# Kernel optimization log

Measured on AMD Instinct MI355X. Metric: run time of the kernel, lower is better.

Reference implementation:

```python
import jax, jax.numpy as jnp
import numpy as np

B = 131072
D = 512


def setup_inputs() -> dict:
    key = jax.random.key(0)
    kx, kL, kb, kc = jax.random.split(key, 4)
    x = jax.random.normal(kx, (B, D), dtype=jnp.float32)
    L = jax.random.normal(kL, (D, D), dtype=jnp.float32)
    b = jax.random.normal(kb, (D,), dtype=jnp.float32)
    c = jax.random.normal(kc, (1,), dtype=jnp.float32)
    return {"x": x, "L": L, "b": b, "c": c}


def reference(x, L, b, c):
    # y = diag(x L L' x') + x b + c == sum((x @ L)**2, -1) + x @ b + c
    # Avoids the naive O(B^2 D) GEMM and O(B^2) intermediate.
    xL = x @ L                      # [B, D]
    quad = jnp.sum(xL * xL, axis=-1)  # [B]
    y = quad + x @ b + c            # [B] (c broadcasts from [1])
    return y[:, None]               # [B, 1]
```

## Files before the change

### kernel.cpp

```cpp
#include <hip/hip_runtime.h>
#include <stdint.h>

#define D_DIM   512
#define BM      64
#define BK      32
#define THREADS 256
#define NBLOCKS 2048

typedef __attribute__((ext_vector_type(8))) __bf16 bf16x8;
typedef __attribute__((ext_vector_type(4))) float  f32x4;

__device__ __forceinline__ unsigned short f32_to_bf16_rne(float f) {
    uint32_t u = __builtin_bit_cast(uint32_t, f);
    u += 0x7FFFu + ((u >> 16) & 1u);
    return (unsigned short)(u >> 16);
}

__global__ void prep_lt(const float* __restrict__ L, unsigned short* __restrict__ Ltf) {
    int o = blockIdx.x * 256 + threadIdx.x;
    #pragma unroll
    for (int i = 0; i < 4; ++i) {
        int idx  = o + i * 65536;
        int e    = idx & 7;
        int l    = (idx >> 3) & 63;
        int tile = idx >> 9;
        int ntg  = tile & 31;
        int ks   = tile >> 5;
        int n    = ntg * 16 + (l & 15);
        int k    = ks * 32 + (l >> 4) * 8 + e;
        Ltf[idx] = f32_to_bf16_rne(L[k * 512 + n]);
    }
}

__global__ __launch_bounds__(THREADS, 2)
void psd_main(const float* __restrict__ x, const unsigned short* __restrict__ Ltf,
              const float* __restrict__ b, const float* __restrict__ c,
              float* __restrict__ out) {
    __shared__ __align__(16) float As[3][BM * BK];
    __shared__ __align__(16) float bsh[D_DIM];
    __shared__ float wpart[4][BM];
    __shared__ float bpart[BM];

    const int t    = threadIdx.x;
    const int w    = t >> 6;
    const int lane = t & 63;
    const int g    = lane >> 4;
    const int ln   = lane & 15;
    const int r8   = lane >> 3;
    const int u8   = lane & 7;

    char* AsB  = (char*)&As[0][0];
    char* bshB = (char*)&bsh[0];
    const char* xB = (const char*)x + (size_t)blockIdx.x * (BM * 2048);

    const unsigned short* LtW = Ltf + (size_t)w * 4096 + (size_t)lane * 8;

    f32x4 acc[4][8];
    #pragma unroll
    for (int m = 0; m < 4; ++m)
        #pragma unroll
        for (int nt = 0; nt < 8; ++nt)
            acc[m][nt] = (f32x4){0.f, 0.f, 0.f, 0.f};
    float bacc = 0.f;

#define STAGE(QOFF, SL)                                                                  \
    {                                                                                    \
        char* ldsw = AsB + (SL) * 8192 + w * 2048;                                       \
        _Pragma("unroll")                                                                \
        for (int j = 0; j < 2; ++j) {                                                    \
            const int row = w * 16 + j * 8 + r8;                                         \
            const char* gsrc = xB + (size_t)row * 2048 + (QOFF)                          \
                             + ((u8 ^ (row & 7)) << 4);                                  \
            __builtin_amdgcn_global_load_lds(                                            \
                (const __attribute__((address_space(1))) void*)gsrc,                     \
                (__attribute__((address_space(3))) void*)(ldsw + j * 1024), 16, 0, 0);   \
        }                                                                                \
    }

#define COMPUTE(RB)                                                                      \
    {                                                                                    \
        _Pragma("unroll")                                                                \
        for (int m = 0; m < 4; ++m) {                                                    \
            const int row = m * 16 + ln;                                                 \
            const int cb  = g * 2;                                                       \
            f32x4 f0 = *(const f32x4*)((RB) + row * 128 + (((cb    ) ^ (row & 7)) << 4));\
            f32x4 f1 = *(const f32x4*)((RB) + row * 128 + (((cb + 1) ^ (row & 7)) << 4));\
            bf16x8 a;                                                                    \
            a[0] = (__bf16)f0[0]; a[1] = (__bf16)f0[1];                                  \
            a[2] = (__bf16)f0[2]; a[3] = (__bf16)f0[3];                                  \
            a[4] = (__bf16)f1[0]; a[5] = (__bf16)f1[1];                                  \
            a[6] = (__bf16)f1[2]; a[7] = (__bf16)f1[3];                                  \
            _Pragma("unroll")                                                            \
            for (int nt = 0; nt < 8; ++nt)                                               \
                acc[m][nt] = __builtin_amdgcn_mfma_f32_16x16x32_bf16(a, bfr[nt], acc[m][nt], 0, 0, 0); \
        }                                                                                \
    }

#define XB(RB, BOFF)                                                                     \
    {                                                                                    \
        const int row = t >> 2;                                                          \
        const int rsw = row & 7;                                                         \
        _Pragma("unroll")                                                                \
        for (int i = 0; i < 2; ++i) {                                                    \
            const int unit = (t & 3) * 2 + i;                                            \
            f32x4 xv = *(const f32x4*)((RB) + row * 128 + ((unit ^ rsw) << 4));          \
            f32x4 bv = *(const f32x4*)(bshB + (BOFF) + unit * 16);                       \
            bacc += xv[0] * bv[0] + xv[1] * bv[1] + xv[2] * bv[2] + xv[3] * bv[3];       \
        }                                                                                \
    }

    if (t < 128) {
        const char* gsrc = (const char*)b + (size_t)t * 16;
        __builtin_amdgcn_global_load_lds(
            (const __attribute__((address_space(1))) void*)gsrc,
            (__attribute__((address_space(3))) void*)(bshB + t * 16), 16, 0, 0);
    }
    STAGE(0, 0)
    STAGE(128, 1)
    asm volatile("s_waitcnt vmcnt(2)" ::: "memory");
    __builtin_amdgcn_s_barrier();

    int sl   = 0;
    int qoff = 2 * 128;
    int boff = 0;
    const unsigned short* Lp = LtW;

    #pragma unroll 1
    for (int q = 0; q < 14; ++q) {
        bf16x8 bfr[8];
        #pragma unroll
        for (int nt = 0; nt < 8; ++nt)
            bfr[nt] = *(const bf16x8*)(Lp + nt * 512);
        __builtin_amdgcn_sched_barrier(0);

        int sls = sl + 2; if (sls >= 3) sls -= 3;
        STAGE(qoff, sls)

        const char* rb = AsB + sl * 8192;
        COMPUTE(rb)
        XB(rb, boff)

        asm volatile("s_waitcnt lgkmcnt(0)" ::: "memory");
        asm volatile("s_waitcnt vmcnt(2)" ::: "memory");
        __builtin_amdgcn_s_barrier();

        if (++sl == 3) sl = 0;
        qoff += 128;
        boff += 128;
        Lp   += 16384;
    }

    {
        bf16x8 bfr[8];
        #pragma unroll
        for (int nt = 0; nt < 8; ++nt)
            bfr[nt] = *(const bf16x8*)(Lp + nt * 512);
        const char* rb = AsB + 2 * 8192;
        COMPUTE(rb)
        XB(rb, 14 * 128)
        asm volatile("s_waitcnt lgkmcnt(0)" ::: "memory");
        asm volatile("s_waitcnt vmcnt(0)" ::: "memory");
        __builtin_amdgcn_s_barrier();
    }
    {
        bf16x8 bfr[8];
        #pragma unroll
        for (int nt = 0; nt < 8; ++nt)
            bfr[nt] = *(const bf16x8*)(Lp + 16384 + nt * 512);
        const char* rb = AsB;
        COMPUTE(rb)
        XB(rb, 15 * 128)
    }

#undef STAGE
#undef COMPUTE
#undef XB

    #pragma unroll
    for (int m = 0; m < 4; ++m) {
        #pragma unroll
        for (int r = 0; r < 4; ++r) {
            float s = 0.f;
            #pragma unroll
            for (int nt = 0; nt < 8; ++nt) { float vv = acc[m][nt][r]; s += vv * vv; }
            s += __shfl_xor(s, 1);
            s += __shfl_xor(s, 2);
            s += __shfl_xor(s, 4);
            s += __shfl_xor(s, 8);
            if (ln == 0) wpart[w][m * 16 + g * 4 + r] = s;
        }
    }

    {
        float s = bacc;
        s += __shfl_xor(s, 1);
        s += __shfl_xor(s, 2);
        if ((lane & 3) == 0) bpart[t >> 2] = s;
    }
    __syncthreads();

    if (t < BM) {
        float y = c[0] + bpart[t]
                + wpart[0][t] + wpart[1][t] + wpart[2][t] + wpart[3][t];
        out[(size_t)blockIdx.x * BM + t] = y;
    }
}

extern "C" void kernel_launch(void* const* d_in, const int* in_sizes, int n_in,
                              void* d_out, int out_size, void* d_ws, size_t ws_size,
                              hipStream_t stream) {
    const float* x = (const float*)d_in[0];
    const float* L = (const float*)d_in[1];
    const float* b = (const float*)d_in[2];
    const float* c = (const float*)d_in[3];
    float* out = (float*)d_out;
    unsigned short* Ltf = (unsigned short*)d_ws;

    prep_lt<<<256, 256, 0, stream>>>(L, Ltf);
    psd_main<<<NBLOCKS, THREADS, 0, stream>>>(x, Ltf, b, c, out);
}
```

Measured before the change: 100.7 us.

## Convert x tiles to bf16 once into a shared ring and software-pipeline L loads

Each K-tile of x is now converted from fp32 to bf16 a single time by a cooperative pass, fused with the x·b dot product, and written into a swizzled double-buffered bf16 LDS ring. The MFMA loop then reads bf16 fragments directly instead of every wave re-reading and re-converting fp32 rows. L fragment loads are split into halves and prefetched one stage ahead, and the x staging is deepened to three tiles in flight. This removes redundant conversion ALU work and LDS traffic. It adds more LDS, hand-tuned waitcnt values that must match the load counts, and a longer unrolled prologue and epilogue.

```diff
diff --git a/kernel.cpp b/kernel.cpp
--- a/kernel.cpp
+++ b/kernel.cpp
@@ -3,7 +3,6 @@
 
 #define D_DIM   512
 #define BM      64
-#define BK      32
 #define THREADS 256
 #define NBLOCKS 2048
 
@@ -36,7 +35,8 @@
 void psd_main(const float* __restrict__ x, const unsigned short* __restrict__ Ltf,
               const float* __restrict__ b, const float* __restrict__ c,
               float* __restrict__ out) {
-    __shared__ __align__(16) float As[3][BM * BK];
+    __shared__ __align__(16) float pad[3][BM * 32];
+    __shared__ __align__(16) unsigned short ringb[2][BM * 32];
     __shared__ __align__(16) float bsh[D_DIM];
     __shared__ float wpart[4][BM];
     __shared__ float bpart[BM];
@@ -48,11 +48,13 @@
     const int ln   = lane & 15;
     const int r8   = lane >> 3;
     const int u8   = lane & 7;
-
-    char* AsB  = (char*)&As[0][0];
+    const int crow = t >> 2;
+    const int ccg  = t & 3;
+
+    char* padB = (char*)&pad[0][0];
+    char* rngB = (char*)&ringb[0][0];
     char* bshB = (char*)&bsh[0];
     const char* xB = (const char*)x + (size_t)blockIdx.x * (BM * 2048);
-
     const unsigned short* LtW = Ltf + (size_t)w * 4096 + (size_t)lane * 8;
 
     f32x4 acc[4][8];
@@ -63,118 +65,142 @@
             acc[m][nt] = (f32x4){0.f, 0.f, 0.f, 0.f};
     float bacc = 0.f;
 
-#define STAGE(QOFF, SL)                                                                  \
-    {                                                                                    \
-        char* ldsw = AsB + (SL) * 8192 + w * 2048;                                       \
+#define STAGE(K, SOFF)                                                                   \
+    {                                                                                    \
+        char* ldsw = padB + (SOFF) + w * 2048;                                           \
         _Pragma("unroll")                                                                \
         for (int j = 0; j < 2; ++j) {                                                    \
             const int row = w * 16 + j * 8 + r8;                                         \
-            const char* gsrc = xB + (size_t)row * 2048 + (QOFF)                          \
-                             + ((u8 ^ (row & 7)) << 4);                                  \
+            const char* gsrc = xB + (size_t)row * 2048 + (K) * 128 + ((u8 ^ r8) << 4);   \
             __builtin_amdgcn_global_load_lds(                                            \
                 (const __attribute__((address_space(1))) void*)gsrc,                     \
                 (__attribute__((address_space(3))) void*)(ldsw + j * 1024), 16, 0, 0);   \
         }                                                                                \
     }
 
-#define COMPUTE(RB)                                                                      \
+#define CVT_XB(K, COFF, ROFF)                                                            \
+    {                                                                                    \
+        const char* ps = padB + (COFF);                                                  \
+        f32x4 e0 = *(const f32x4*)(ps + crow * 128 + (((ccg * 2    ) ^ (crow & 7)) << 4)); \
+        f32x4 e1 = *(const f32x4*)(ps + crow * 128 + (((ccg * 2 + 1) ^ (crow & 7)) << 4)); \
+        f32x4 b0 = *(const f32x4*)(bshB + (K) * 128 + ccg * 32);                         \
+        f32x4 b1 = *(const f32x4*)(bshB + (K) * 128 + ccg * 32 + 16);                    \
+        bacc += e0[0]*b0[0] + e0[1]*b0[1] + e0[2]*b0[2] + e0[3]*b0[3]                    \
+              + e1[0]*b1[0] + e1[1]*b1[1] + e1[2]*b1[2] + e1[3]*b1[3];                   \
+        bf16x8 hv;                                                                       \
+        hv[0]=(__bf16)e0[0]; hv[1]=(__bf16)e0[1]; hv[2]=(__bf16)e0[2]; hv[3]=(__bf16)e0[3]; \
+        hv[4]=(__bf16)e1[0]; hv[5]=(__bf16)e1[1]; hv[6]=(__bf16)e1[2]; hv[7]=(__bf16)e1[3]; \
+        *(bf16x8*)(rngB + (ROFF) + crow * 64 + ((ccg ^ (crow & 3)) << 4)) = hv;          \
+    }
+
+#define LOADB(DST, Q, H)                                                                 \
+    {                                                                                    \
+        _Pragma("unroll")                                                                \
+        for (int i = 0; i < 4; ++i)                                                      \
+            (DST)[i] = *(const bf16x8*)(LtW + (size_t)(Q) * 16384 + ((H) * 4 + i) * 512); \
+    }
+
+#define COMPUTE_H(ROFF, BS, NB)                                                          \
     {                                                                                    \
         _Pragma("unroll")                                                                \
         for (int m = 0; m < 4; ++m) {                                                    \
             const int row = m * 16 + ln;                                                 \
-            const int cb  = g * 2;                                                       \
-            f32x4 f0 = *(const f32x4*)((RB) + row * 128 + (((cb    ) ^ (row & 7)) << 4));\
-            f32x4 f1 = *(const f32x4*)((RB) + row * 128 + (((cb + 1) ^ (row & 7)) << 4));\
-            bf16x8 a;                                                                    \
-            a[0] = (__bf16)f0[0]; a[1] = (__bf16)f0[1];                                  \
-            a[2] = (__bf16)f0[2]; a[3] = (__bf16)f0[3];                                  \
-            a[4] = (__bf16)f1[0]; a[5] = (__bf16)f1[1];                                  \
-            a[6] = (__bf16)f1[2]; a[7] = (__bf16)f1[3];                                  \
+            bf16x8 a = *(const bf16x8*)(rngB + (ROFF) + row * 64 + ((g ^ (row & 3)) << 4)); \
             _Pragma("unroll")                                                            \
-            for (int nt = 0; nt < 8; ++nt)                                               \
-                acc[m][nt] = __builtin_amdgcn_mfma_f32_16x16x32_bf16(a, bfr[nt], acc[m][nt], 0, 0, 0); \
+            for (int nt = 0; nt < 4; ++nt)                                               \
+                acc[m][(NB) + nt] = __builtin_amdgcn_mfma_f32_16x16x32_bf16(a, (BS)[nt], acc[m][(NB) + nt], 0, 0, 0); \
         }                                                                                \
     }
 
-#define XB(RB, BOFF)                                                                     \
-    {                                                                                    \
-        const int row = t >> 2;                                                          \
-        const int rsw = row & 7;                                                         \
-        _Pragma("unroll")                                                                \
-        for (int i = 0; i < 2; ++i) {                                                    \
-            const int unit = (t & 3) * 2 + i;                                            \
-            f32x4 xv = *(const f32x4*)((RB) + row * 128 + ((unit ^ rsw) << 4));          \
-            f32x4 bv = *(const f32x4*)(bshB + (BOFF) + unit * 16);                       \
-            bacc += xv[0] * bv[0] + xv[1] * bv[1] + xv[2] * bv[2] + xv[3] * bv[3];       \
-        }                                                                                \
-    }
-
-    if (t < 128) {
-        const char* gsrc = (const char*)b + (size_t)t * 16;
+    if (lane < 32) {
+        const char* gsrc = (const char*)b + (size_t)(w * 512 + lane * 16);
         __builtin_amdgcn_global_load_lds(
             (const __attribute__((address_space(1))) void*)gsrc,
-            (__attribute__((address_space(3))) void*)(bshB + t * 16), 16, 0, 0);
+            (__attribute__((address_space(3))) void*)(bshB + w * 512 + lane * 16), 16, 0, 0);
     }
     STAGE(0, 0)
-    STAGE(128, 1)
-    asm volatile("s_waitcnt vmcnt(2)" ::: "memory");
-    __builtin_amdgcn_s_barrier();
-
-    int sl   = 0;
-    int qoff = 2 * 128;
-    int boff = 0;
+    STAGE(1, 8192)
+    STAGE(2, 16384)
+    asm volatile("s_waitcnt vmcnt(4)" ::: "memory");
+    __builtin_amdgcn_s_barrier();
+
+    bf16x8 blo0[4], blo1[4], bhi0[4], bhi1[4];
+    LOADB(blo0, 0, 0)
+    LOADB(blo1, 1, 0)
+    LOADB(bhi0, 0, 1)
+    CVT_XB(0, 0, 0)
+    asm volatile("s_waitcnt lgkmcnt(0)" ::: "memory");
+    __builtin_amdgcn_s_barrier();
+
+    int soff = 0;
+    int coff = 8192;
+    int sK   = 3;
+    int cK   = 1;
     const unsigned short* Lp = LtW;
 
     #pragma unroll 1
-    for (int q = 0; q < 14; ++q) {
-        bf16x8 bfr[8];
-        #pragma unroll
-        for (int nt = 0; nt < 8; ++nt)
-            bfr[nt] = *(const bf16x8*)(Lp + nt * 512);
-        __builtin_amdgcn_sched_barrier(0);
-
-        int sls = sl + 2; if (sls >= 3) sls -= 3;
-        STAGE(qoff, sls)
-
-        const char* rb = AsB + sl * 8192;
-        COMPUTE(rb)
-        XB(rb, boff)
-
+    for (int qp = 0; qp < 6; ++qp) {
+        LOADB(bhi1, (Lp - LtW) / 8192 + 1, 1)
+        STAGE(sK, soff)
+        COMPUTE_H(0, blo0, 0)
+        LOADB(blo0, (Lp - LtW) / 8192 + 2, 0)
+        COMPUTE_H(0, bhi0, 4)
+        asm volatile("s_waitcnt vmcnt(10)" ::: "memory");
+        CVT_XB(cK, coff, 4096)
         asm volatile("s_waitcnt lgkmcnt(0)" ::: "memory");
-        asm volatile("s_waitcnt vmcnt(2)" ::: "memory");
         __builtin_amdgcn_s_barrier();
-
-        if (++sl == 3) sl = 0;
-        qoff += 128;
-        boff += 128;
-        Lp   += 16384;
-    }
-
-    {
-        bf16x8 bfr[8];
-        #pragma unroll
-        for (int nt = 0; nt < 8; ++nt)
-            bfr[nt] = *(const bf16x8*)(Lp + nt * 512);
-        const char* rb = AsB + 2 * 8192;
-        COMPUTE(rb)
-        XB(rb, 14 * 128)
+        soff = (soff == 16384) ? 0 : soff + 8192;
+        coff = (coff == 16384) ? 0 : coff + 8192;
+        ++sK; ++cK; Lp += 8192;
+
+        LOADB(bhi0, (Lp - LtW) / 8192 + 1, 1)
+        STAGE(sK, soff)
+        COMPUTE_H(4096, blo1, 0)
+        LOADB(blo1, (Lp - LtW) / 8192 + 2, 0)
+        COMPUTE_H(4096, bhi1, 4)
+        asm volatile("s_waitcnt vmcnt(10)" ::: "memory");
+        CVT_XB(cK, coff, 0)
         asm volatile("s_waitcnt lgkmcnt(0)" ::: "memory");
-        asm volatile("s_waitcnt vmcnt(0)" ::: "memory");
         __builtin_amdgcn_s_barrier();
-    }
-    {
-        bf16x8 bfr[8];
-        #pragma unroll
-        for (int nt = 0; nt < 8; ++nt)
-            bfr[nt] = *(const bf16x8*)(Lp + 16384 + nt * 512);
-        const char* rb = AsB;
-        COMPUTE(rb)
-        XB(rb, 15 * 128)
-    }
+        soff = (soff == 16384) ? 0 : soff + 8192;
+        coff = (coff == 16384) ? 0 : coff + 8192;
+        ++sK; ++cK; Lp += 8192;
+    }
+
+    LOADB(bhi1, 13, 1)
+    STAGE(15, 0)
+    COMPUTE_H(0, blo0, 0)
+    LOADB(blo0, 14, 0)
+    COMPUTE_H(0, bhi0, 4)
+    asm volatile("s_waitcnt vmcnt(10)" ::: "memory");
+    CVT_XB(13, 8192, 4096)
+    asm volatile("s_waitcnt lgkmcnt(0)" ::: "memory");
+    __builtin_amdgcn_s_barrier();
+
+    LOADB(bhi0, 14, 1)
+    COMPUTE_H(4096, blo1, 0)
+    LOADB(blo1, 15, 0)
+    COMPUTE_H(4096, bhi1, 4)
+    asm volatile("s_waitcnt vmcnt(8)" ::: "memory");
+    CVT_XB(14, 16384, 0)
+    asm volatile("s_waitcnt lgkmcnt(0)" ::: "memory");
+    __builtin_amdgcn_s_barrier();
+
+    LOADB(bhi1, 15, 1)
+    COMPUTE_H(0, blo0, 0)
+    COMPUTE_H(0, bhi0, 4)
+    asm volatile("s_waitcnt vmcnt(4)" ::: "memory");
+    CVT_XB(15, 0, 4096)
+    asm volatile("s_waitcnt lgkmcnt(0)" ::: "memory");
+    __builtin_amdgcn_s_barrier();
+
+    COMPUTE_H(4096, blo1, 0)
+    COMPUTE_H(4096, bhi1, 4)
 
 #undef STAGE
-#undef COMPUTE
-#undef XB
+#undef CVT_XB
+#undef LOADB
+#undef COMPUTE_H
 
     #pragma unroll
     for (int m = 0; m < 4; ++m) {
@@ -195,7 +221,7 @@
         float s = bacc;
         s += __shfl_xor(s, 1);
         s += __shfl_xor(s, 2);
-        if ((lane & 3) == 0) bpart[t >> 2] = s;
+        if ((lane & 3) == 0) bpart[crow] = s;
     }
     __syncthreads();
 
```

Result: slower. 124.1 us (+23.3%).

## Replace barrier-synced triple buffer with 6-slot LDS ring using spin-wait counters

Applied to the files above, without the earlier changes.

Swaps the 3-stage LDS buffer and per-iteration s_barrier for a 6-slot ring. Waves coordinate through shared-memory staged/consumed counters, bumped with atomics and polled in spin loops, so waves no longer run in lockstep. The L-fragment loads are now double-buffered in registers, and COMPUTE raises wave priority via s_setprio. This aims to hide global-load latency with a deeper prefetch and remove barrier stalls. In exchange it adds LDS use, which may cut occupancy, adds spin-wait overhead, and brings ordering risk from relying on vmcnt waits plus LDS flags.

```diff
diff --git a/kernel.cpp b/kernel.cpp
--- a/kernel.cpp
+++ b/kernel.cpp
@@ -3,9 +3,10 @@
 
 #define D_DIM   512
 #define BM      64
-#define BK      32
 #define THREADS 256
 #define NBLOCKS 2048
+#define RING    6
+#define SLOT    8192
 
 typedef __attribute__((ext_vector_type(8))) __bf16 bf16x8;
 typedef __attribute__((ext_vector_type(4))) float  f32x4;
@@ -36,8 +37,10 @@
 void psd_main(const float* __restrict__ x, const unsigned short* __restrict__ Ltf,
               const float* __restrict__ b, const float* __restrict__ c,
               float* __restrict__ out) {
-    __shared__ __align__(16) float As[3][BM * BK];
+    __shared__ __align__(16) float ring[RING * BM * 32];
     __shared__ __align__(16) float bsh[D_DIM];
+    __shared__ unsigned staged[16];
+    __shared__ unsigned consumed[16];
     __shared__ float wpart[4][BM];
     __shared__ float bpart[BM];
 
@@ -49,11 +52,15 @@
     const int r8   = lane >> 3;
     const int u8   = lane & 7;
 
-    char* AsB  = (char*)&As[0][0];
-    char* bshB = (char*)&bsh[0];
+    char* ringB = (char*)&ring[0];
+    char* bshB  = (char*)&bsh[0];
     const char* xB = (const char*)x + (size_t)blockIdx.x * (BM * 2048);
-
     const unsigned short* LtW = Ltf + (size_t)w * 4096 + (size_t)lane * 8;
+
+    volatile unsigned* vst = staged;
+    volatile unsigned* vco = consumed;
+    if (t < 16) { staged[t] = 0; consumed[t] = 0; }
+    __syncthreads();
 
     f32x4 acc[4][8];
     #pragma unroll
@@ -63,28 +70,35 @@
             acc[m][nt] = (f32x4){0.f, 0.f, 0.f, 0.f};
     float bacc = 0.f;
 
-#define STAGE(QOFF, SL)                                                                  \
-    {                                                                                    \
-        char* ldsw = AsB + (SL) * 8192 + w * 2048;                                       \
+#define STAGE(K, SOFF)                                                                   \
+    {                                                                                    \
+        char* ldsw = ringB + (SOFF) + w * 2048;                                          \
         _Pragma("unroll")                                                                \
         for (int j = 0; j < 2; ++j) {                                                    \
-            const int row = w * 16 + j * 8 + r8;                                         \
-            const char* gsrc = xB + (size_t)row * 2048 + (QOFF)                          \
-                             + ((u8 ^ (row & 7)) << 4);                                  \
+            const char* gsrc = xB + (size_t)(w * 16 + j * 8 + r8) * 2048 + (K) * 128     \
+                             + ((u8 ^ r8) << 4);                                         \
             __builtin_amdgcn_global_load_lds(                                            \
                 (const __attribute__((address_space(1))) void*)gsrc,                     \
                 (__attribute__((address_space(3))) void*)(ldsw + j * 1024), 16, 0, 0);   \
         }                                                                                \
     }
 
-#define COMPUTE(RB)                                                                      \
-    {                                                                                    \
+#define LOADB(DST, Q)                                                                    \
+    {                                                                                    \
+        _Pragma("unroll")                                                                \
+        for (int i = 0; i < 8; ++i)                                                      \
+            (DST)[i] = *(const bf16x8*)(LtW + (size_t)(Q) * 16384 + i * 512);            \
+    }
+
+#define COMPUTE(RBOFF)                                                                   \
+    {                                                                                    \
+        __builtin_amdgcn_s_setprio(1);                                                   \
         _Pragma("unroll")                                                                \
         for (int m = 0; m < 4; ++m) {                                                    \
             const int row = m * 16 + ln;                                                 \
-            const int cb  = g * 2;                                                       \
-            f32x4 f0 = *(const f32x4*)((RB) + row * 128 + (((cb    ) ^ (row & 7)) << 4));\
-            f32x4 f1 = *(const f32x4*)((RB) + row * 128 + (((cb + 1) ^ (row & 7)) << 4));\
+            const char* rp = ringB + (RBOFF) + row * 128;                                \
+            f32x4 f0 = *(const f32x4*)(rp + (((g * 2    ) ^ (ln & 7)) << 4));            \
+            f32x4 f1 = *(const f32x4*)(rp + (((g * 2 + 1) ^ (ln & 7)) << 4));            \
             bf16x8 a;                                                                    \
             a[0] = (__bf16)f0[0]; a[1] = (__bf16)f0[1];                                  \
             a[2] = (__bf16)f0[2]; a[3] = (__bf16)f0[3];                                  \
@@ -92,90 +106,104 @@
             a[6] = (__bf16)f1[2]; a[7] = (__bf16)f1[3];                                  \
             _Pragma("unroll")                                                            \
             for (int nt = 0; nt < 8; ++nt)                                               \
-                acc[m][nt] = __builtin_amdgcn_mfma_f32_16x16x32_bf16(a, bfr[nt], acc[m][nt], 0, 0, 0); \
+                acc[m][nt] = __builtin_amdgcn_mfma_f32_16x16x32_bf16(a, bcur[nt], acc[m][nt], 0, 0, 0); \
         }                                                                                \
-    }
-
-#define XB(RB, BOFF)                                                                     \
+        __builtin_amdgcn_s_setprio(0);                                                   \
+    }
+
+#define XB(RBOFF, BOFF)                                                                  \
     {                                                                                    \
         const int row = t >> 2;                                                          \
-        const int rsw = row & 7;                                                         \
         _Pragma("unroll")                                                                \
         for (int i = 0; i < 2; ++i) {                                                    \
             const int unit = (t & 3) * 2 + i;                                            \
-            f32x4 xv = *(const f32x4*)((RB) + row * 128 + ((unit ^ rsw) << 4));          \
+            f32x4 xv = *(const f32x4*)(ringB + (RBOFF) + row * 128 + ((unit ^ (row & 7)) << 4)); \
             f32x4 bv = *(const f32x4*)(bshB + (BOFF) + unit * 16);                       \
             bacc += xv[0] * bv[0] + xv[1] * bv[1] + xv[2] * bv[2] + xv[3] * bv[3];       \
         }                                                                                \
     }
 
-    if (t < 128) {
-        const char* gsrc = (const char*)b + (size_t)t * 16;
+#define BUMP(ARR, IDX) if (lane == 0) atomicAdd((unsigned*)&(ARR)[(IDX)], 1u);
+#define SWAPB() { _Pragma("unroll") for (int i = 0; i < 8; ++i) bcur[i] = bnxt[i]; }
+
+    if (lane < 32) {
+        const char* gsrc = (const char*)b + (size_t)(w * 512 + lane * 16);
         __builtin_amdgcn_global_load_lds(
             (const __attribute__((address_space(1))) void*)gsrc,
-            (__attribute__((address_space(3))) void*)(bshB + t * 16), 16, 0, 0);
-    }
-    STAGE(0, 0)
-    STAGE(128, 1)
-    asm volatile("s_waitcnt vmcnt(2)" ::: "memory");
-    __builtin_amdgcn_s_barrier();
-
-    int sl   = 0;
-    int qoff = 2 * 128;
-    int boff = 0;
-    const unsigned short* Lp = LtW;
-
-    #pragma unroll 1
-    for (int q = 0; q < 14; ++q) {
-        bf16x8 bfr[8];
-        #pragma unroll
-        for (int nt = 0; nt < 8; ++nt)
-            bfr[nt] = *(const bf16x8*)(Lp + nt * 512);
-        __builtin_amdgcn_sched_barrier(0);
-
-        int sls = sl + 2; if (sls >= 3) sls -= 3;
-        STAGE(qoff, sls)
-
-        const char* rb = AsB + sl * 8192;
-        COMPUTE(rb)
-        XB(rb, boff)
-
-        asm volatile("s_waitcnt lgkmcnt(0)" ::: "memory");
-        asm volatile("s_waitcnt vmcnt(2)" ::: "memory");
-        __builtin_amdgcn_s_barrier();
-
-        if (++sl == 3) sl = 0;
-        qoff += 128;
-        boff += 128;
-        Lp   += 16384;
-    }
+            (__attribute__((address_space(3))) void*)(bshB + w * 512 + lane * 16), 16, 0, 0);
+    }
+    bf16x8 bcur[8], bnxt[8];
+    LOADB(bcur, 0)
+    STAGE(0, 0) STAGE(1, 8192) STAGE(2, 16384) STAGE(3, 24576) STAGE(4, 32768)
+
+    STAGE(5, 40960)
+    LOADB(bnxt, 1)
+    asm volatile("s_waitcnt vmcnt(10)" ::: "memory");
+    BUMP(staged, 0) BUMP(staged, 1) BUMP(staged, 2) BUMP(staged, 3) BUMP(staged, 4)
+    while (vst[0] < 4u) ;
+    COMPUTE(0)
+    XB(0, 0)
+    asm volatile("s_waitcnt lgkmcnt(0)" ::: "memory");
+    BUMP(consumed, 0)
+    SWAPB()
 
     {
-        bf16x8 bfr[8];
-        #pragma unroll
-        for (int nt = 0; nt < 8; ++nt)
-            bfr[nt] = *(const bf16x8*)(Lp + nt * 512);
-        const char* rb = AsB + 2 * 8192;
-        COMPUTE(rb)
-        XB(rb, 14 * 128)
-        asm volatile("s_waitcnt lgkmcnt(0)" ::: "memory");
-        asm volatile("s_waitcnt vmcnt(0)" ::: "memory");
-        __builtin_amdgcn_s_barrier();
-    }
-    {
-        bf16x8 bfr[8];
-        #pragma unroll
-        for (int nt = 0; nt < 8; ++nt)
-            bfr[nt] = *(const bf16x8*)(Lp + 16384 + nt * 512);
-        const char* rb = AsB;
-        COMPUTE(rb)
-        XB(rb, 15 * 128)
-    }
-
+        int rbOff = 8192;
+        int stOff = 0;
+        int boff  = 128;
+        const unsigned short* Lp = LtW + 2 * 16384;
+
+        #pragma unroll 1
+        for (int q = 1; q <= 10; ++q) {
+            while (vco[q - 1] < 4u) ;
+            STAGE(q + 5, stOff)
+            #pragma unroll
+            for (int i = 0; i < 8; ++i)
+                bnxt[i] = *(const bf16x8*)(Lp + i * 512);
+            asm volatile("s_waitcnt vmcnt(10)" ::: "memory");
+            BUMP(staged, q + 4)
+            while (vst[q] < 4u) ;
+            COMPUTE(rbOff)
+            XB(rbOff, boff)
+            asm volatile("s_waitcnt lgkmcnt(0)" ::: "memory");
+            BUMP(consumed, q)
+            SWAPB()
+            rbOff += 8192; if (rbOff == RING * SLOT) rbOff = 0;
+            stOff += 8192; if (stOff == RING * SLOT) stOff = 0;
+            boff  += 128;
+            Lp    += 16384;
+        }
+    }
+
+#define TAIL(Q, RBOFF, HASB, VM)                                                         \
+    {                                                                                    \
+        if (HASB) LOADB(bnxt, (Q) + 1)                                                   \
+        asm volatile("s_waitcnt vmcnt(" #VM ")" ::: "memory");                           \
+        while (vst[(Q)] < 4u) ;                                                          \
+        COMPUTE(RBOFF)                                                                   \
+        XB(RBOFF, (Q) * 128)                                                             \
+        SWAPB()                                                                          \
+    }
+    if (lane == 0) atomicAdd((unsigned*)&staged[15], 1u);
+    asm volatile("s_waitcnt vmcnt(8)" ::: "memory");
+    while (vst[11] < 4u) ;
+    COMPUTE(40960)
+    XB(40960, 11 * 128)
+    LOADB(bnxt, 12)
+    SWAPB()
+    TAIL(12, 0,     1, 8)
+    TAIL(13, 8192,  1, 8)
+    TAIL(14, 16384, 1, 8)
+    TAIL(15, 24576, 0, 0)
+#undef TAIL
 #undef STAGE
+#undef LOADB
 #undef COMPUTE
 #undef XB
-
+#undef BUMP
+#undef SWAPB
+
+    __syncthreads();
     #pragma unroll
     for (int m = 0; m < 4; ++m) {
         #pragma unroll
@@ -190,7 +218,6 @@
             if (ln == 0) wpart[w][m * 16 + g * 4 + r] = s;
         }
     }
-
     {
         float s = bacc;
         s += __shfl_xor(s, 1);
```

Result: slower. 162.5 us (+61.4%).
